# Kernel optimization log

Hardware: AMD Instinct MI355X
Metric: run time of the kernel (lower is better)

The kernel has to match this reference:

```python
import jax, jax.numpy as jnp
import numpy as np

INS, OUTS = 768, 64
B, S = 8, 2048


def setup_inputs() -> dict:
    key = jax.random.key(0)
    ks = jax.random.split(key, 7)
    scale = 1.0 / np.sqrt(INS)
    inputs = jax.random.normal(ks[0], (B, S, INS), dtype=jnp.float32)
    Wq = jax.random.uniform(ks[1], (INS, OUTS), jnp.float32, -scale, scale)
    bq = jax.random.uniform(ks[2], (OUTS,), jnp.float32, -scale, scale)
    Wk = jax.random.uniform(ks[3], (INS, OUTS), jnp.float32, -scale, scale)
    bk = jax.random.uniform(ks[4], (OUTS,), jnp.float32, -scale, scale)
    Wv = jax.random.uniform(ks[5], (INS, OUTS), jnp.float32, -scale, scale)
    bv = jax.random.uniform(ks[6], (OUTS,), jnp.float32, -scale, scale)
    return {"inputs": inputs, "Wq": Wq, "bq": bq, "Wk": Wk, "bk": bk, "Wv": Wv, "bv": bv}


def reference(inputs, Wq, bq, Wk, bk, Wv, bv):
    # QKV projections: [B, S, ins] @ [ins, outs] -> [B, S, outs]
    q = jnp.einsum('bsi,io->bso', inputs, Wq) + bq
    k = jnp.einsum('bsi,io->bso', inputs, Wk) + bk
    v = jnp.einsum('bsi,io->bso', inputs, Wv) + bv
    dim_k = k.shape[-1]
    # scores: [B, S, S] (materialized, as in the original bmm-based impl)
    att = jnp.einsum('bqd,bkd->bqk', q, k) / jnp.sqrt(jnp.asarray(dim_k, q.dtype))
    att_soft = jax.nn.softmax(att, axis=-1)
    out = jnp.einsum('bqk,bkd->bqd', att_soft, v)
    return out
```

## Files before the change

### kernel.cpp

```cpp
#include <hip/hip_runtime.h>
#include <hip/hip_bf16.h>
#include <stdint.h>

#define INS 768
#define OUTS 64
#define BB 8
#define SS 2048
#define LDP 40

typedef __attribute__((ext_vector_type(8))) short short8;
typedef __attribute__((ext_vector_type(4))) float f32x4;

__device__ inline unsigned short f2bf(float f) {
  union { float f; uint32_t u; } v; v.f = f;
  uint32_t r = v.u + 0x7FFFu + ((v.u >> 16) & 1u);
  return (unsigned short)(r >> 16);
}

__device__ inline short8 cvt8hw(float4 a, float4 b) {
  union { __hip_bfloat162 h[4]; short8 s; } u;
  u.h[0] = __float22bfloat162_rn(make_float2(a.x, a.y));
  u.h[1] = __float22bfloat162_rn(make_float2(a.z, a.w));
  u.h[2] = __float22bfloat162_rn(make_float2(b.x, b.y));
  u.h[3] = __float22bfloat162_rn(make_float2(b.z, b.w));
  return u.s;
}

__device__ inline void gl_lds16(const void* g, void* l) {
  __builtin_amdgcn_global_load_lds(
      (const __attribute__((address_space(1))) uint32_t*)g,
      (__attribute__((address_space(3))) uint32_t*)l, 16, 0, 0);
}

__global__ __launch_bounds__(256) void prep(
    const float* __restrict__ Wq, const float* __restrict__ Wk,
    const float* __restrict__ Wv, unsigned short* __restrict__ WT) {
  const int idx = blockIdx.x * 256 + threadIdx.x;
  const int m = idx / (INS * OUTS);
  const int r = idx - m * (INS * OUTS);
  const int k = r >> 6, n = r & 63;
  const float* W = (m == 0) ? Wq : (m == 1) ? Wk : Wv;
  const float s = (m == 0) ? 0.125f : 1.0f;
  WT[((size_t)m * OUTS + n) * INS + k] = f2bf(W[(size_t)k * OUTS + n] * s);
}

__global__ __launch_bounds__(256) void qkv(
    const float* __restrict__ X, const unsigned short* __restrict__ WT,
    const float* __restrict__ bq, const float* __restrict__ bk,
    const float* __restrict__ bv,
    unsigned short* __restrict__ Qg, unsigned short* __restrict__ Kg,
    unsigned short* __restrict__ Vtg) {
  __shared__ __align__(16) float Xs[2][1024];
  const int tid  = threadIdx.x;
  const int wave = tid >> 6, lane = tid & 63;
  const int quad = lane >> 4, l16 = lane & 15;
  const int chg  = wave;
  const int row0 = blockIdx.x * 32;

  const int sr = tid >> 3, ss = tid & 7;
  const char* gsrc =
      (const char*)(X + (size_t)(row0 + sr) * INS) + ((ss ^ (sr & 7)) << 4);
  char* ldst = (char*)&Xs[0][0] + wave * 1024;

  const float* Bm[3]; float scl[3]; int col0[3];
  const unsigned short* Wt[3];
#pragma unroll
  for (int nt = 0; nt < 3; ++nt) {
    const int n0 = chg * 48 + nt * 16;
    const int mat = n0 >> 6;
    col0[nt] = n0 & 63;
    Wt[nt] = WT + ((size_t)mat * OUTS + col0[nt] + l16) * INS + quad * 8;
    if (mat == 0)      { Bm[nt] = bq; scl[nt] = 0.125f; }
    else if (mat == 1) { Bm[nt] = bk; scl[nt] = 1.0f; }
    else               { Bm[nt] = bv; scl[nt] = 1.0f; }
  }

  int off0[2], off1[2];
#pragma unroll
  for (int fr = 0; fr < 2; ++fr) {
    const int lr = fr * 16 + l16;
    off0[fr] = lr * 128 + ((((quad << 1)    ) ^ (lr & 7)) << 4);
    off1[fr] = lr * 128 + ((((quad << 1) | 1) ^ (lr & 7)) << 4);
  }

  f32x4 acc[2][3];
#pragma unroll
  for (int fr = 0; fr < 2; ++fr)
#pragma unroll
    for (int nt = 0; nt < 3; ++nt) acc[fr][nt] = (f32x4){0.f, 0.f, 0.f, 0.f};

  short8 wb[2][3];

  gl_lds16(gsrc, ldst);
#pragma unroll
  for (int nt = 0; nt < 3; ++nt)
    wb[0][nt] = *reinterpret_cast<const short8*>(Wt[nt]);
  __syncthreads();

#pragma unroll
  for (int kc = 0; kc < 24; ++kc) {
    const int cur = kc & 1;
    if (kc + 1 < 24) {
      gl_lds16(gsrc + (size_t)(kc + 1) * 128, ldst + ((cur ^ 1) << 12));
#pragma unroll
      for (int nt = 0; nt < 3; ++nt)
        wb[(kc + 1) & 1][nt] =
            *reinterpret_cast<const short8*>(Wt[nt] + (kc + 1) * 32);
    }
    const char* xb = (const char*)&Xs[cur][0];
    float4 f00 = *reinterpret_cast<const float4*>(xb + off0[0]);
    float4 f01 = *reinterpret_cast<const float4*>(xb + off1[0]);
    float4 f10 = *reinterpret_cast<const float4*>(xb + off0[1]);
    float4 f11 = *reinterpret_cast<const float4*>(xb + off1[1]);
    short8 a0 = cvt8hw(f00, f01);
    short8 a1 = cvt8hw(f10, f11);
#pragma unroll
    for (int nt = 0; nt < 3; ++nt) {
      acc[0][nt] = __builtin_amdgcn_mfma_f32_16x16x32_bf16(a0, wb[cur][nt], acc[0][nt], 0, 0, 0);
      acc[1][nt] = __builtin_amdgcn_mfma_f32_16x16x32_bf16(a1, wb[cur][nt], acc[1][nt], 0, 0, 0);
    }
    __syncthreads();
  }

#pragma unroll
  for (int fr = 0; fr < 2; ++fr) {
    const int gm0 = row0 + fr * 16 + quad * 4;
#pragma unroll
    for (int nt = 0; nt < 3; ++nt) {
      const int n = chg * 48 + nt * 16 + l16;
      const float bias = Bm[nt][col0[nt] + l16] * scl[nt];
      if (n < 128) {
        unsigned short* dstbase = (n < 64) ? Qg : Kg;
        const int nn = n & 63;
#pragma unroll
        for (int r = 0; r < 4; ++r)
          dstbase[(size_t)(gm0 + r) * OUTS + nn] = f2bf(acc[fr][nt][r] + bias);
      } else {
        const int d = n - 128;
        const int batch = gm0 >> 11, s0 = gm0 & 2047;
        ushort4 pk;
        pk.x = f2bf(acc[fr][nt][0] + bias);
        pk.y = f2bf(acc[fr][nt][1] + bias);
        pk.z = f2bf(acc[fr][nt][2] + bias);
        pk.w = f2bf(acc[fr][nt][3] + bias);
        *reinterpret_cast<ushort4*>(&Vtg[((size_t)batch * OUTS + d) * SS + s0]) = pk;
      }
    }
  }
}

__global__ __launch_bounds__(256) void attn(
    const unsigned short* __restrict__ Qg, const unsigned short* __restrict__ Kg,
    const unsigned short* __restrict__ Vtg,
    float* __restrict__ OP, float* __restrict__ LS) {
  __shared__ __align__(16) char KsB[2][4096];
  __shared__ __align__(16) char VsB[2][4096];
  __shared__ __align__(16) unsigned short Ps[4][2][16 * LDP];
  const int tid  = threadIdx.x;
  const int wave = tid >> 6, lane = tid & 63;
  const int quad = lane >> 4, l16 = lane & 15;
  const int bt  = blockIdx.x >> 6;
  const int rem = blockIdx.x & 63;
  const int qb  = rem >> 2, ksl = rem & 3;
  const int q0 = qb * 128 + wave * 32;
  const unsigned short* Qb = Qg + (size_t)bt * SS * OUTS;
  const unsigned short* Kb = Kg + (size_t)bt * SS * OUTS;
  const unsigned short* Vb = Vtg + (size_t)bt * OUTS * SS;
  const int jbeg = ksl * 512;

  const int krow = wave * 8 + (lane >> 3), ks8 = lane & 7;
  const int vrow = wave * 16 + (lane >> 2), vs4 = lane & 3;
  const int vsw  = (vrow & 3) ^ ((vrow >> 2) & 3);
  const char* ksrc = (const char*)(Kb + (size_t)(jbeg + krow) * OUTS) +
                     ((ks8 ^ (krow & 7)) << 4);
  const char* vsrc = (const char*)(Vb + (size_t)vrow * SS + jbeg) +
                     ((vs4 ^ vsw) << 4);

  short8 aq[2][2];
#pragma unroll
  for (int mh = 0; mh < 2; ++mh)
#pragma unroll
    for (int ks = 0; ks < 2; ++ks)
      aq[mh][ks] = *reinterpret_cast<const short8*>(
          Qb + (size_t)(q0 + mh * 16 + l16) * OUTS + ks * 32 + quad * 8);

  int koff[2][2];
#pragma unroll
  for (int nt2 = 0; nt2 < 2; ++nt2)
#pragma unroll
    for (int ks = 0; ks < 2; ++ks)
      koff[nt2][ks] = (nt2 * 16 + l16) * 128 +
                      ((((ks << 2) | quad) ^ (l16 & 7)) << 4);
  int voff[4];
#pragma unroll
  for (int nt = 0; nt < 4; ++nt) {
    const int dr = nt * 16 + l16;
    voff[nt] = dr * 64 + ((quad ^ ((dr & 3) ^ ((dr >> 2) & 3))) << 4);
  }

  f32x4 oacc[2][4];
#pragma unroll
  for (int mh = 0; mh < 2; ++mh)
#pragma unroll
    for (int nt = 0; nt < 4; ++nt) oacc[mh][nt] = (f32x4){0.f, 0.f, 0.f, 0.f};
  float lsum[2][4] = {{0.f,0.f,0.f,0.f},{0.f,0.f,0.f,0.f}};

  gl_lds16(ksrc, &KsB[0][0] + wave * 1024);
  gl_lds16(vsrc, &VsB[0][0] + wave * 1024);
  __syncthreads();

  for (int kc = 0; kc < 16; ++kc) {
    const int cur = kc & 1;
    if (kc + 1 < 16) {
      gl_lds16(ksrc + (size_t)(kc + 1) * 4096, &KsB[cur ^ 1][0] + wave * 1024);
      gl_lds16(vsrc + (size_t)(kc + 1) * 64,   &VsB[cur ^ 1][0] + wave * 1024);
    }
    const char* kb8 = &KsB[cur][0];
    const char* vb8 = &VsB[cur][0];
    short8 bk[2][2], bv[4];
#pragma unroll
    for (int nt2 = 0; nt2 < 2; ++nt2)
#pragma unroll
      for (int ks = 0; ks < 2; ++ks)
        bk[nt2][ks] = *reinterpret_cast<const short8*>(kb8 + koff[nt2][ks]);
#pragma unroll
    for (int nt = 0; nt < 4; ++nt)
      bv[nt] = *reinterpret_cast<const short8*>(vb8 + voff[nt]);

#pragma unroll
    for (int mh = 0; mh < 2; ++mh) {
      f32x4 sc[2];
      sc[0] = (f32x4){0.f,0.f,0.f,0.f}; sc[1] = (f32x4){0.f,0.f,0.f,0.f};
#pragma unroll
      for (int ks = 0; ks < 2; ++ks)
#pragma unroll
        for (int nt2 = 0; nt2 < 2; ++nt2)
          sc[nt2] = __builtin_amdgcn_mfma_f32_16x16x32_bf16(aq[mh][ks], bk[nt2][ks], sc[nt2], 0, 0, 0);

      unsigned short* Pw = Ps[wave][mh];
#pragma unroll
      for (int nt2 = 0; nt2 < 2; ++nt2)
#pragma unroll
        for (int r = 0; r < 4; ++r) {
          float p = __expf(sc[nt2][r]);
          lsum[mh][r] += p;
          Pw[(quad * 4 + r) * LDP + nt2 * 16 + l16] = f2bf(p);
        }
      short8 ap = *reinterpret_cast<const short8*>(&Pw[l16 * LDP + quad * 8]);
#pragma unroll
      for (int nt = 0; nt < 4; ++nt)
        oacc[mh][nt] = __builtin_amdgcn_mfma_f32_16x16x32_bf16(ap, bv[nt], oacc[mh][nt], 0, 0, 0);
    }
    __syncthreads();
  }

#pragma unroll
  for (int st = 1; st < 16; st <<= 1)
#pragma unroll
    for (int mh = 0; mh < 2; ++mh)
#pragma unroll
      for (int r = 0; r < 4; ++r) lsum[mh][r] += __shfl_xor(lsum[mh][r], st, 64);

  float* OPb = OP + ((size_t)ksl * BB + bt) * SS * OUTS;
#pragma unroll
  for (int mh = 0; mh < 2; ++mh)
#pragma unroll
    for (int nt = 0; nt < 4; ++nt)
#pragma unroll
      for (int r = 0; r < 4; ++r) {
        int q = q0 + mh * 16 + quad * 4 + r;
        OPb[(size_t)q * OUTS + nt * 16 + l16] = oacc[mh][nt][r];
      }
  if (l16 == 0) {
#pragma unroll
    for (int mh = 0; mh < 2; ++mh)
#pragma unroll
      for (int r = 0; r < 4; ++r)
        LS[(size_t)ksl * BB * SS + bt * SS + q0 + mh * 16 + quad * 4 + r] = lsum[mh][r];
  }
}

__global__ __launch_bounds__(256) void combine(
    const float* __restrict__ OP, const float* __restrict__ LS,
    float* __restrict__ out) {
  const size_t i4 = (size_t)blockIdx.x * 256 + threadIdx.x;
  const size_t row = (i4 * 4) >> 6;
  float4 o = make_float4(0.f, 0.f, 0.f, 0.f);
  float l = 0.f;
#pragma unroll
  for (int ks = 0; ks < 4; ++ks) {
    float4 t = reinterpret_cast<const float4*>(OP + (size_t)ks * BB * SS * OUTS)[i4];
    o.x += t.x; o.y += t.y; o.z += t.z; o.w += t.w;
    l += LS[(size_t)ks * BB * SS + row];
  }
  const float inv = 1.0f / l;
  reinterpret_cast<float4*>(out)[i4] = make_float4(o.x * inv, o.y * inv, o.z * inv, o.w * inv);
}

extern "C" void kernel_launch(void* const* d_in, const int* in_sizes, int n_in,
                              void* d_out, int out_size, void* d_ws, size_t ws_size,
                              hipStream_t stream) {
  const float* X  = (const float*)d_in[0];
  const float* Wq = (const float*)d_in[1];
  const float* bq = (const float*)d_in[2];
  const float* Wk = (const float*)d_in[3];
  const float* bk = (const float*)d_in[4];
  const float* Wv = (const float*)d_in[5];
  const float* bv = (const float*)d_in[6];
  float* out = (float*)d_out;

  char* ws = (char*)d_ws;
  unsigned short* Qg  = (unsigned short*)(ws);
  unsigned short* Kg  = (unsigned short*)(ws + (size_t)2 * 1024 * 1024);
  unsigned short* Vtg = (unsigned short*)(ws + (size_t)4 * 1024 * 1024);
  unsigned short* WT  = (unsigned short*)(ws + (size_t)6 * 1024 * 1024);
  float*          OP  = (float*)(ws + (size_t)7 * 1024 * 1024);
  float*          LS  = (float*)(ws + (size_t)23 * 1024 * 1024);

  prep<<<576, 256, 0, stream>>>(Wq, Wk, Wv, WT);
  qkv<<<512, 256, 0, stream>>>(X, WT, bq, bk, bv, Qg, Kg, Vtg);
  attn<<<512, 256, 0, stream>>>(Qg, Kg, Vtg, OP, LS);
  combine<<<1024, 256, 0, stream>>>(OP, LS, out);
}
```

Measured before the change: 144.1 us.

## Deepen LDS prefetch to four-stage ring with manual vmcnt barriers

Both the QKV projection and attention kernels move from a double-buffered LDS scheme to a four-slot ring with a prefetch distance of three tiles. The weight registers become a three-slot rotation. Each iteration now uses one explicit `s_waitcnt vmcnt(N)` plus barrier instead of two `__syncthreads`, so more global-to-LDS loads stay in flight while MFMA work proceeds. The cost is twice the LDS footprint, which may lower occupancy. Correctness also depends on the hand-counted vmcnt values matching the number of outstanding loads issued per iteration.

```diff
diff --git a/kernel.cpp b/kernel.cpp
--- a/kernel.cpp
+++ b/kernel.cpp
@@ -31,6 +31,15 @@
       (const __attribute__((address_space(1))) uint32_t*)g,
       (__attribute__((address_space(3))) uint32_t*)l, 16, 0, 0);
 }
+
+__device__ inline void memfence_sched() { asm volatile("" ::: "memory"); }
+
+#define PIPE_BARRIER(N)                                        \
+  do {                                                         \
+    asm volatile("s_waitcnt vmcnt(" #N ")" ::: "memory");      \
+    __builtin_amdgcn_s_barrier();                              \
+    __builtin_amdgcn_sched_barrier(0);                         \
+  } while (0)
 
 __global__ __launch_bounds__(256) void prep(
     const float* __restrict__ Wq, const float* __restrict__ Wk,
@@ -50,7 +59,7 @@
     const float* __restrict__ bv,
     unsigned short* __restrict__ Qg, unsigned short* __restrict__ Kg,
     unsigned short* __restrict__ Vtg) {
-  __shared__ __align__(16) float Xs[2][1024];
+  __shared__ __align__(16) float Xs[4][1024];
   const int tid  = threadIdx.x;
   const int wave = tid >> 6, lane = tid & 63;
   const int quad = lane >> 4, l16 = lane & 15;
@@ -60,7 +69,7 @@
   const int sr = tid >> 3, ss = tid & 7;
   const char* gsrc =
       (const char*)(X + (size_t)(row0 + sr) * INS) + ((ss ^ (sr & 7)) << 4);
-  char* ldst = (char*)&Xs[0][0] + wave * 1024;
+  char* ldsb = (char*)&Xs[0][0] + wave * 1024;
 
   const float* Bm[3]; float scl[3]; int col0[3];
   const unsigned short* Wt[3];
@@ -89,25 +98,26 @@
 #pragma unroll
     for (int nt = 0; nt < 3; ++nt) acc[fr][nt] = (f32x4){0.f, 0.f, 0.f, 0.f};
 
-  short8 wb[2][3];
-
-  gl_lds16(gsrc, ldst);
+  short8 wb[3][3];
+
+  gl_lds16(gsrc, ldsb);
 #pragma unroll
   for (int nt = 0; nt < 3; ++nt)
     wb[0][nt] = *reinterpret_cast<const short8*>(Wt[nt]);
-  __syncthreads();
+  memfence_sched();
+  gl_lds16(gsrc + 128, ldsb + 4096);
+  gl_lds16(gsrc + 256, ldsb + 8192);
+#pragma unroll
+  for (int nt = 0; nt < 3; ++nt)
+    wb[1][nt] = *reinterpret_cast<const short8*>(Wt[nt] + 32);
 
 #pragma unroll
   for (int kc = 0; kc < 24; ++kc) {
-    const int cur = kc & 1;
-    if (kc + 1 < 24) {
-      gl_lds16(gsrc + (size_t)(kc + 1) * 128, ldst + ((cur ^ 1) << 12));
-#pragma unroll
-      for (int nt = 0; nt < 3; ++nt)
-        wb[(kc + 1) & 1][nt] =
-            *reinterpret_cast<const short8*>(Wt[nt] + (kc + 1) * 32);
-    }
-    const char* xb = (const char*)&Xs[cur][0];
+    if (kc <= 21)      PIPE_BARRIER(4);
+    else if (kc == 22) PIPE_BARRIER(3);
+    else               PIPE_BARRIER(0);
+
+    const char* xb = (const char*)&Xs[kc & 3][0];
     float4 f00 = *reinterpret_cast<const float4*>(xb + off0[0]);
     float4 f01 = *reinterpret_cast<const float4*>(xb + off1[0]);
     float4 f10 = *reinterpret_cast<const float4*>(xb + off0[1]);
@@ -116,10 +126,17 @@
     short8 a1 = cvt8hw(f10, f11);
 #pragma unroll
     for (int nt = 0; nt < 3; ++nt) {
-      acc[0][nt] = __builtin_amdgcn_mfma_f32_16x16x32_bf16(a0, wb[cur][nt], acc[0][nt], 0, 0, 0);
-      acc[1][nt] = __builtin_amdgcn_mfma_f32_16x16x32_bf16(a1, wb[cur][nt], acc[1][nt], 0, 0, 0);
-    }
-    __syncthreads();
+      acc[0][nt] = __builtin_amdgcn_mfma_f32_16x16x32_bf16(a0, wb[kc % 3][nt], acc[0][nt], 0, 0, 0);
+      acc[1][nt] = __builtin_amdgcn_mfma_f32_16x16x32_bf16(a1, wb[kc % 3][nt], acc[1][nt], 0, 0, 0);
+    }
+    if (kc + 3 < 24)
+      gl_lds16(gsrc + (size_t)(kc + 3) * 128, ldsb + (size_t)((kc + 3) & 3) * 4096);
+    if (kc + 2 < 24) {
+#pragma unroll
+      for (int nt = 0; nt < 3; ++nt)
+        wb[(kc + 2) % 3][nt] =
+            *reinterpret_cast<const short8*>(Wt[nt] + (kc + 2) * 32);
+    }
   }
 
 #pragma unroll
@@ -153,8 +170,8 @@
     const unsigned short* __restrict__ Qg, const unsigned short* __restrict__ Kg,
     const unsigned short* __restrict__ Vtg,
     float* __restrict__ OP, float* __restrict__ LS) {
-  __shared__ __align__(16) char KsB[2][4096];
-  __shared__ __align__(16) char VsB[2][4096];
+  __shared__ __align__(16) char KsB[4][4096];
+  __shared__ __align__(16) char VsB[4][4096];
   __shared__ __align__(16) unsigned short Ps[4][2][16 * LDP];
   const int tid  = threadIdx.x;
   const int wave = tid >> 6, lane = tid & 63;
@@ -205,18 +222,22 @@
     for (int nt = 0; nt < 4; ++nt) oacc[mh][nt] = (f32x4){0.f, 0.f, 0.f, 0.f};
   float lsum[2][4] = {{0.f,0.f,0.f,0.f},{0.f,0.f,0.f,0.f}};
 
-  gl_lds16(ksrc, &KsB[0][0] + wave * 1024);
-  gl_lds16(vsrc, &VsB[0][0] + wave * 1024);
-  __syncthreads();
-
+  memfence_sched();
+  gl_lds16(ksrc,                      &KsB[0][0] + wave * 1024);
+  gl_lds16(vsrc,                      &VsB[0][0] + wave * 1024);
+  gl_lds16(ksrc + (size_t)1 * 4096,   &KsB[1][0] + wave * 1024);
+  gl_lds16(vsrc + (size_t)1 * 64,     &VsB[1][0] + wave * 1024);
+  gl_lds16(ksrc + (size_t)2 * 4096,   &KsB[2][0] + wave * 1024);
+  gl_lds16(vsrc + (size_t)2 * 64,     &VsB[2][0] + wave * 1024);
+
+#pragma unroll
   for (int kc = 0; kc < 16; ++kc) {
-    const int cur = kc & 1;
-    if (kc + 1 < 16) {
-      gl_lds16(ksrc + (size_t)(kc + 1) * 4096, &KsB[cur ^ 1][0] + wave * 1024);
-      gl_lds16(vsrc + (size_t)(kc + 1) * 64,   &VsB[cur ^ 1][0] + wave * 1024);
-    }
-    const char* kb8 = &KsB[cur][0];
-    const char* vb8 = &VsB[cur][0];
+    if (kc <= 13)      PIPE_BARRIER(4);
+    else if (kc == 14) PIPE_BARRIER(2);
+    else               PIPE_BARRIER(0);
+
+    const char* kb8 = &KsB[kc & 3][0];
+    const char* vb8 = &VsB[kc & 3][0];
     short8 bk[2][2], bv[4];
 #pragma unroll
     for (int nt2 = 0; nt2 < 2; ++nt2)
@@ -251,7 +272,11 @@
       for (int nt = 0; nt < 4; ++nt)
         oacc[mh][nt] = __builtin_amdgcn_mfma_f32_16x16x32_bf16(ap, bv[nt], oacc[mh][nt], 0, 0, 0);
     }
-    __syncthreads();
+
+    if (kc + 3 < 16) {
+      gl_lds16(ksrc + (size_t)(kc + 3) * 4096, &KsB[(kc + 3) & 3][0] + wave * 1024);
+      gl_lds16(vsrc + (size_t)(kc + 3) * 64,   &VsB[(kc + 3) & 3][0] + wave * 1024);
+    }
   }
 
 #pragma unroll
```

Measured after the change: 138.4 us. 1.04x faster.
